# Optimization experiments

Hardware: AMD Instinct MI355X
Metric: run time of the kernel (lower is better)

The kernel has to match this reference:

```python
import jax, jax.numpy as jnp
import numpy as np

D = 256          # d_embed
KD = 256         # key_d_embed
NHEAD = 8
DK = D // NHEAD  # 32
QH = QW = 128
QWS = 16
KH = KW = 64
KWS = 8
R = QWS // KWS   # qk_ratio = 2
SCALE = 1.0 / np.sqrt(DK)


def _rel_index():
    # query coords on fine grid, key coords scaled up by ratio R
    qc = np.stack(np.meshgrid(np.arange(QWS), np.arange(QWS), indexing='ij'), -1).reshape(-1, 2)
    kc = np.stack(np.meshgrid(np.arange(KWS), np.arange(KWS), indexing='ij'), -1).reshape(-1, 2) * R
    rel = qc[:, None, :] - kc[None, :, :] + (QWS - R)  # values in [0, 2*QWS-R-1]
    return jnp.asarray(rel[..., 0] * (2 * QWS - R) + rel[..., 1])  # (QWS^2, KWS^2)


def _partition(t, ws):
    # (B, h, H, W, d) -> (B, h, H/ws, W/ws, ws*ws, d)
    B, h, H, W, d = t.shape
    t = t.reshape(B, h, H // ws, ws, W // ws, ws, d).transpose(0, 1, 2, 4, 3, 5, 6)
    return t.reshape(B, h, H // ws, W // ws, ws * ws, d)


def _merge(t, ws, H, W):
    # inverse of _partition
    B, h, nH, nW, _, d = t.shape
    t = t.reshape(B, h, nH, nW, ws, ws, d).transpose(0, 1, 2, 4, 3, 5, 6)
    return t.reshape(B, h, H, W, d)


def setup_inputs() -> dict:
    key = jax.random.key(0)
    ks = jax.random.split(key, 9)
    x = jax.random.normal(ks[0], (8, QH, QW, D), dtype=jnp.float32)
    z = jax.random.normal(ks[1], (8, KH, KW, KD), dtype=jnp.float32)
    mask = jax.random.randint(ks[2], (1, NHEAD, QH // QWS, QW // QWS, QWS * QWS, KWS * KWS), 0, 2) == 1
    Wq = jax.random.normal(ks[3], (D, D), dtype=jnp.float32) * 0.02
    bq = jnp.zeros((D,), dtype=jnp.float32)
    Wkv = jax.random.normal(ks[4], (KD, 2 * D), dtype=jnp.float32) * 0.02
    bkv = jnp.zeros((2 * D,), dtype=jnp.float32)
    Wo = jax.random.normal(ks[5], (D, D), dtype=jnp.float32) * 0.02
    bo = jnp.zeros((D,), dtype=jnp.float32)
    rel_table = jax.random.normal(ks[6], ((2 * QWS - R) ** 2, NHEAD), dtype=jnp.float32) * 0.02
    return {"x": x, "z": z, "mask": mask, "Wq": Wq, "bq": bq, "Wkv": Wkv, "bkv": bkv, "Wo": Wo, "bo": bo, "rel_table": rel_table}


def reference(x, z, mask, Wq, bq, Wkv, bkv, Wo, bo, rel_table):
    B, H, W, _ = x.shape
    q = (x @ Wq + bq).reshape(B, H, W, NHEAD, DK).transpose(0, 3, 1, 2, 4)        # (B,h,H,W,dk)
    kv = (z @ Wkv + bkv).reshape(B, KH, KW, 2, NHEAD, DK).transpose(3, 0, 4, 1, 2, 5)
    k, v = kv[0], kv[1]                                                           # (B,h,_H,_W,dk)
    sq, sk = QWS // 2, KWS // 2
    q = jnp.roll(q, (-sq, -sq), axis=(2, 3))
    k = jnp.roll(k, (-sk, -sk), axis=(2, 3))
    v = jnp.roll(v, (-sk, -sk), axis=(2, 3))
    q = _partition(q, QWS)   # (B,h,nh,nw,QWS^2,dk)
    k = _partition(k, KWS)   # (B,h,nh,nw,KWS^2,dk)
    v = _partition(v, KWS)
    attn = jnp.einsum('bhnmqd,bhnmkd->bhnmqk', q, k) * SCALE
    bias = rel_table[_rel_index()].transpose(2, 0, 1)[None, :, None, None]        # (1,h,1,1,QWS^2,KWS^2)
    attn = attn + bias
    attn = jnp.where(mask, jnp.float32(-1e9), attn)
    attn = jax.nn.softmax(attn, axis=-1)
    out = jnp.einsum('bhnmqk,bhnmkd->bhnmqd', attn, v)
    out = _merge(out, QWS, H, W)
    out = jnp.roll(out, (sq, sq), axis=(2, 3))
    out = out.transpose(0, 2, 3, 1, 4).reshape(B, H, W, D)
    return out @ Wo + bo
```

## Files before the change

kernel.cpp:

```cpp
#include <hip/hip_runtime.h>
#include <hip/hip_bf16.h>
#include <type_traits>


typedef __attribute__((ext_vector_type(8))) short short8v;
typedef __attribute__((ext_vector_type(4))) float f32x4;
typedef __attribute__((ext_vector_type(8))) unsigned short ushort8v;
typedef unsigned long long u64;

#define DEV __device__ __forceinline__

DEV unsigned short f2bf(float f) {
    union { float f; unsigned u; } v; v.f = f;
    unsigned r = v.u + 0x7FFFu + ((v.u >> 16) & 1u);
    return (unsigned short)(r >> 16);
}

DEV short8v cvt_f32x8(const float4 lo, const float4 hi) {
    union U { __hip_bfloat162 h[4]; short8v s; } u;
    u.h[0] = __float22bfloat162_rn(float2{lo.x, lo.y});
    u.h[1] = __float22bfloat162_rn(float2{lo.z, lo.w});
    u.h[2] = __float22bfloat162_rn(float2{hi.x, hi.y});
    u.h[3] = __float22bfloat162_rn(float2{hi.z, hi.w});
    return u.s;
}

DEV uint2 pack4(f32x4 v) {
    union { __hip_bfloat162 h; unsigned u; } a, b;
    a.h = __float22bfloat162_rn(float2{v[0], v[1]});
    b.h = __float22bfloat162_rn(float2{v[2], v[3]});
    return uint2{a.u, b.u};
}

#define ATT_SCALE 0.17677669529663687f

__global__ void prep_weights(const float* __restrict__ Wq, const float* __restrict__ Wkv,
                             const float* __restrict__ Wo,
                             unsigned short* __restrict__ WqT, unsigned short* __restrict__ WkvT,
                             unsigned short* __restrict__ WoT) {
    int idx = blockIdx.x * 256 + threadIdx.x;
    if (idx < 65536) {
        int n = idx >> 8, k = idx & 255;
        WqT[idx] = f2bf(Wq[k * 256 + n] * ATT_SCALE);
    } else if (idx < 196608) {
        int i = idx - 65536;
        int n = i >> 8, k = i & 255;
        WkvT[i] = f2bf(Wkv[k * 512 + n]);
    } else {
        int i = idx - 196608;
        int n = i >> 8, k = i & 255;
        WoT[i] = f2bf(Wo[k * 256 + n]);
    }
}

__global__ void prep_bias(const float* __restrict__ rel_table, const float* __restrict__ bq,
                          float* __restrict__ biasb, float* __restrict__ bqs) {
    int idx = blockIdx.x * 256 + threadIdx.x;
    if (idx < 131072) {
        int head = idx >> 14;
        int q = (idx >> 6) & 255;
        int k = idx & 63;
        int qi = q >> 4, qj = q & 15;
        int ki = k >> 3, kj = k & 7;
        int r0 = qi - 2 * ki + 14, r1 = qj - 2 * kj + 14;
        biasb[idx] = rel_table[(r0 * 30 + r1) * 8 + head];
    } else if (idx < 131328) {
        int i = idx - 131072;
        bqs[i] = bq[i] * ATT_SCALE;
    }
}

__global__ void prep_mask(const int* __restrict__ mask, u64* __restrict__ mp) {
    int idx = blockIdx.x * 256 + threadIdx.x;
    const int4* src = reinterpret_cast<const int4*>(mask + (size_t)idx * 64);
    u64 bits = 0;
#pragma unroll
    for (int c = 0; c < 16; ++c) {
        int4 v = src[c];
        if (v.x) bits |= 1ull << (c * 4 + 0);
        if (v.y) bits |= 1ull << (c * 4 + 1);
        if (v.z) bits |= 1ull << (c * 4 + 2);
        if (v.w) bits |= 1ull << (c * 4 + 3);
    }
    mp[idx] = bits;
}

__global__ __launch_bounds__(512, 2) void gemm_rs(
    const unsigned short* __restrict__ A,
    const unsigned short* __restrict__ WT,
    const float* __restrict__ bias, float* __restrict__ out)
{
    __shared__ __align__(16) unsigned char R[131072];

    const int tid = threadIdx.x;
    const int w = tid >> 6, lane = tid & 63, lr = lane & 15, lg = lane >> 4;
    const int g = w >> 2, wn = (w & 3) * 64;
    const size_t rowbase = (size_t)blockIdx.x * 512 + (size_t)g * 256;

    short8v wf[8][4];
#pragma unroll
    for (int kt = 0; kt < 8; ++kt)
#pragma unroll
        for (int nt = 0; nt < 4; ++nt)
            wf[kt][nt] = *reinterpret_cast<const short8v*>(
                WT + (size_t)(wn + nt * 16 + lr) * 256 + kt * 32 + lg * 8);

    const int r_ = lane >> 5;
    const int u_ = lane & 31;
    unsigned char* ringbase = R + w * 16384;
    const unsigned char* Ab = (const unsigned char*)A;

    auto issue = [&](int t, int slot) {
        size_t gbyte0 = (rowbase + (size_t)t * 16) * 512;
        unsigned char* ldst = ringbase + slot * 8192;
#pragma unroll
        for (int c = 0; c < 8; ++c) {
            int r = 2 * c + r_;
            int v = u_ ^ r;
            __builtin_amdgcn_global_load_lds(
                (const __attribute__((address_space(1))) void*)
                    (Ab + gbyte0 + (size_t)r * 512 + v * 16),
                (__attribute__((address_space(3))) void*)(ldst + c * 1024),
                16, 0, 0);
        }
    };

    issue(0, 0);

    for (int t = 0; t < 16; ++t) {
        const int slot = t & 1;
        if (t == 0) asm volatile("s_waitcnt vmcnt(0)" ::: "memory");
        else        asm volatile("s_waitcnt vmcnt(4)" ::: "memory");
        __builtin_amdgcn_sched_barrier(0);

        short8v af[8];
#pragma unroll
        for (int kt = 0; kt < 8; ++kt)
            af[kt] = *reinterpret_cast<const short8v*>(
                ringbase + slot * 8192 + lr * 512 + (((kt * 4 + lg) ^ lr) << 4));
        __builtin_amdgcn_sched_barrier(0);

        if (t + 1 < 16) issue(t + 1, slot ^ 1);

        f32x4 acc[4];
#pragma unroll
        for (int nt = 0; nt < 4; ++nt) acc[nt] = {0.f, 0.f, 0.f, 0.f};
#pragma unroll
        for (int kt = 0; kt < 8; ++kt)
#pragma unroll
            for (int nt = 0; nt < 4; ++nt)
                acc[nt] = __builtin_amdgcn_mfma_f32_16x16x32_bf16(
                    wf[kt][nt], af[kt], acc[nt], 0, 0, 0);

        size_t row = rowbase + (size_t)t * 16 + lr;
#pragma unroll
        for (int nt = 0; nt < 4; ++nt) {
            f32x4 b4 = *reinterpret_cast<const f32x4*>(bias + wn + nt * 16 + lg * 4);
            *reinterpret_cast<f32x4*>(out + row * 256 + wn + nt * 16 + lg * 4)
                = acc[nt] + b4;
        }
    }
}

template <bool AF32, bool OUT_BF16>
__global__ __launch_bounds__(512, 2) void gemm_ws(
    const void* __restrict__ Ain, const unsigned short* __restrict__ BT,
    const float* __restrict__ bias, void* __restrict__ Cout)
{
    __shared__ __align__(16) unsigned char Wl[131072];
    const float* Af = (const float*)Ain;

    const int tid = threadIdx.x;
    const int w = tid >> 6, lane = tid & 63, lr = lane & 15, lg = lane >> 4;
    const size_t wm = (size_t)blockIdx.x * 512 + w * 64;

    {
        int r = tid >> 1, half = tid & 1;
        const unsigned short* src = BT + r * 256 + half * 128;
        int rsw = (r >> 1) & 3;
#pragma unroll
        for (int kk = 0; kk < 4; ++kk) {
            int kt = half * 4 + kk;
#pragma unroll
            for (int sl = 0; sl < 4; ++sl) {
                ushort8v v = *reinterpret_cast<const ushort8v*>(src + kk * 32 + sl * 8);
                *reinterpret_cast<ushort8v*>(
                    &Wl[kt * 16384 + r * 64 + ((sl ^ rsw) << 4)]) = v;
            }
        }
    }
    __syncthreads();

    const int swzb = (lg ^ ((lr >> 1) & 3)) << 4;
    const int colb = lg * 4;

#define RD_W(kt, nt) (*reinterpret_cast<const short8v*>( \
        &Wl[(kt) * 16384 + ((nt) * 16 + lr) * 64 + swzb]))

#define EPILOGUE(t)                                                             \
    _Pragma("unroll")                                                           \
    for (int nt = 0; nt < 16; ++nt) {                                           \
        f32x4 b4 = *reinterpret_cast<const f32x4*>(bias + nt * 16 + colb);      \
        f32x4 v = acc[nt] + b4;                                                 \
        size_t row = wm + (t) * 16 + lr;                                        \
        if constexpr (OUT_BF16)                                                 \
            *reinterpret_cast<uint2*>(                                          \
                (unsigned short*)Cout + row * 256 + nt * 16 + colb) = pack4(v); \
        else                                                                    \
            *reinterpret_cast<f32x4*>(                                          \
                (float*)Cout + row * 256 + nt * 16 + colb) = v;                 \
    }

    float4 bufA[16], bufB[16];
#define LOADT_F(BUF, t) {                                                       \
        const float* p = Af + (wm + (t) * 16 + lr) * 256 + lg * 8;              \
        _Pragma("unroll")                                                       \
        for (int kt = 0; kt < 8; ++kt) {                                        \
            BUF[kt * 2]     = *reinterpret_cast<const float4*>(p + kt * 32);    \
            BUF[kt * 2 + 1] = *reinterpret_cast<const float4*>(p + kt * 32 + 4);\
        } }
#define COMP_F(BUF, t) {                                                        \
        f32x4 acc[16];                                                          \
        _Pragma("unroll")                                                       \
        for (int nt = 0; nt < 16; ++nt) acc[nt] = {0.f, 0.f, 0.f, 0.f};         \
        _Pragma("unroll")                                                       \
        for (int kt = 0; kt < 8; ++kt) {                                        \
            short8v a = cvt_f32x8(BUF[kt * 2], BUF[kt * 2 + 1]);                \
            _Pragma("unroll")                                                   \
            for (int nt = 0; nt < 16; ++nt)                                     \
                acc[nt] = __builtin_amdgcn_mfma_f32_16x16x32_bf16(              \
                    RD_W(kt, nt), a, acc[nt], 0, 0, 0);                         \
        }                                                                       \
        EPILOGUE(t) }
    LOADT_F(bufA, 0);
    LOADT_F(bufB, 1); COMP_F(bufA, 0);
    LOADT_F(bufA, 2); COMP_F(bufB, 1);
    LOADT_F(bufB, 3); COMP_F(bufA, 2);
    COMP_F(bufB, 3);
#undef LOADT_F
#undef COMP_F
#undef RD_W
#undef EPILOGUE
}

template <bool AF32, bool OUT_BF16>
__global__ __launch_bounds__(256) void gemm_proj(
    const void* __restrict__ Ain, const unsigned short* __restrict__ BT,
    const float* __restrict__ bias, void* __restrict__ Cout,
    int M, int N, int K)
{
    __shared__ __align__(16) unsigned char As[2][8192];
    __shared__ __align__(16) unsigned char Bs[2][8192];
    const float* Af = (const float*)Ain;

    const int tid = threadIdx.x;
    const int mb = blockIdx.y * 128, nb = blockIdx.x * 128;
    const int w = tid >> 6, lane = tid & 63, lr = lane & 15, lg = lane >> 4;
    const int wm = (w >> 1) * 64, wn = (w & 1) * 64;

    const int cr0 = (w << 5) + (lane >> 2);
    const int csp = lane & 3;
    const int cs0 = csp ^ ((cr0 >> 1) & 3);
    const int cs1 = csp ^ (((cr0 + 16) >> 1) & 3);

    auto stageB = [&](int buf, int kb) {
        __builtin_amdgcn_global_load_lds(
            (const __attribute__((address_space(1))) void*)(BT + (size_t)(nb + cr0) * K + kb + cs0 * 8),
            (__attribute__((address_space(3))) void*)(&Bs[buf][w << 11]), 16, 0, 0);
        __builtin_amdgcn_global_load_lds(
            (const __attribute__((address_space(1))) void*)(BT + (size_t)(nb + cr0 + 16) * K + kb + cs1 * 8),
            (__attribute__((address_space(3))) void*)(&Bs[buf][(w << 11) + 1024]), 16, 0, 0);
    };

    float4 areg[2][2];
    auto loadA = [&](int kb) {
#pragma unroll
        for (int i = 0; i < 2; ++i) {
            int flat = tid + (i << 8);
            int r = flat >> 2, sp = flat & 3;
            int s = sp ^ ((r >> 1) & 3);
            const float* src = Af + (size_t)(mb + r) * K + kb + s * 8;
            areg[i][0] = *reinterpret_cast<const float4*>(src);
            areg[i][1] = *reinterpret_cast<const float4*>(src + 4);
        }
    };
    auto writeA = [&](int buf) {
#pragma unroll
        for (int i = 0; i < 2; ++i) {
            int flat = tid + (i << 8);
            int r = flat >> 2, sp = flat & 3;
            ushort8v u = { f2bf(areg[i][0].x), f2bf(areg[i][0].y),
                           f2bf(areg[i][0].z), f2bf(areg[i][0].w),
                           f2bf(areg[i][1].x), f2bf(areg[i][1].y),
                           f2bf(areg[i][1].z), f2bf(areg[i][1].w) };
            *reinterpret_cast<ushort8v*>(&As[buf][r * 64 + sp * 16]) = u;
        }
    };
    auto rdA = [&](int buf, int row) -> short8v {
        int swz = (lg ^ ((row >> 1) & 3)) << 4;
        return *reinterpret_cast<const short8v*>(&As[buf][row * 64 + swz]);
    };
    auto rdB = [&](int buf, int row) -> short8v {
        int swz = (lg ^ ((row >> 1) & 3)) << 4;
        return *reinterpret_cast<const short8v*>(&Bs[buf][row * 64 + swz]);
    };

    f32x4 acc[4][4];
#pragma unroll
    for (int i = 0; i < 4; ++i)
#pragma unroll
        for (int j = 0; j < 4; ++j) acc[i][j] = {0.f, 0.f, 0.f, 0.f};

    loadA(0); stageB(0, 0); writeA(0);
    __syncthreads();

    const int NT = K >> 5;
    int cur = 0;
    for (int t = 0; t < NT; ++t) {
        if (t + 1 < NT) { loadA((t + 1) << 5); stageB(cur ^ 1, (t + 1) << 5); }
        short8v af[4], bfr[4];
#pragma unroll
        for (int mt = 0; mt < 4; ++mt) af[mt] = rdA(cur, wm + mt * 16 + lr);
#pragma unroll
        for (int nt = 0; nt < 4; ++nt) bfr[nt] = rdB(cur, wn + nt * 16 + lr);
#pragma unroll
        for (int mt = 0; mt < 4; ++mt)
#pragma unroll
            for (int nt = 0; nt < 4; ++nt)
                acc[mt][nt] = __builtin_amdgcn_mfma_f32_16x16x32_bf16(
                    af[mt], bfr[nt], acc[mt][nt], 0, 0, 0);
        if (t + 1 < NT) writeA(cur ^ 1);
        __syncthreads();
        cur ^= 1;
    }

#pragma unroll
    for (int mt = 0; mt < 4; ++mt)
#pragma unroll
        for (int nt = 0; nt < 4; ++nt)
#pragma unroll
            for (int j = 0; j < 4; ++j) {
                int row = mb + wm + mt * 16 + lg * 4 + j;
                int col = nb + wn + nt * 16 + lr;
                float v = acc[mt][nt][j] + bias[col];
                if constexpr (OUT_BF16)
                    ((unsigned short*)Cout)[(size_t)row * N + col] = f2bf(v);
                else
                    ((float*)Cout)[(size_t)row * N + col] = v;
            }
}

__global__ __launch_bounds__(256) void win_attn(
    unsigned short* __restrict__ Qbuf,
    const unsigned short* __restrict__ KVbuf,
    const u64* __restrict__ maskp,
    const float* __restrict__ biasb)
{
    __shared__ __align__(16) unsigned char Pb[256 * 128];
    __shared__ __align__(16) unsigned short Vt[32][72];

    const int tid = threadIdx.x;
    const int win = blockIdx.x, head = blockIdx.y, b = blockIdx.z;
    const int wi = win >> 3, wj = win & 7;
    const int w = tid >> 6, lane = tid & 63, lr = lane & 15, lg = lane >> 4;
    const int qb = w * 64;

    {
        int key = tid & 63, c = tid >> 6;
        int kr = (wi * 8 + (key >> 3) + 4) & 63;
        int kc = (wj * 8 + (key & 7) + 4) & 63;
        ushort8v v = *reinterpret_cast<const ushort8v*>(
            KVbuf + ((size_t)(b * 4096 + kr * 64 + kc)) * 512 + 256 + head * 32 + c * 8);
#pragma unroll
        for (int e = 0; e < 8; ++e) Vt[c * 8 + e][key] = v[e];
    }

    short8v qf[4], kf[4];
#pragma unroll
    for (int mt = 0; mt < 4; ++mt) {
        int q = qb + mt * 16 + lr;
        int gr = (wi * 16 + (q >> 4) + 8) & 127;
        int gc = (wj * 16 + (q & 15) + 8) & 127;
        qf[mt] = *reinterpret_cast<const short8v*>(
            Qbuf + ((size_t)(b * 16384 + gr * 128 + gc)) * 256 + head * 32 + lg * 8);
    }
#pragma unroll
    for (int nt = 0; nt < 4; ++nt) {
        int key = nt * 16 + lr;
        int kr = (wi * 8 + (key >> 3) + 4) & 63;
        int kc = (wj * 8 + (key & 7) + 4) & 63;
        kf[nt] = *reinterpret_cast<const short8v*>(
            KVbuf + ((size_t)(b * 4096 + kr * 64 + kc)) * 512 + head * 32 + lg * 8);
    }

    f32x4 s[4][4];
#pragma unroll
    for (int mt = 0; mt < 4; ++mt)
#pragma unroll
        for (int nt = 0; nt < 4; ++nt) s[mt][nt] = {0.f, 0.f, 0.f, 0.f};
    __builtin_amdgcn_s_setprio(1);
#pragma unroll
    for (int mt = 0; mt < 4; ++mt)
#pragma unroll
        for (int nt = 0; nt < 4; ++nt)
            s[mt][nt] = __builtin_amdgcn_mfma_f32_16x16x32_bf16(qf[mt], kf[nt], s[mt][nt], 0, 0, 0);
    __builtin_amdgcn_s_setprio(0);

    const u64* mrow = maskp + (size_t)(head * 64 + win) * 256;
#pragma unroll
    for (int mt = 0; mt < 4; ++mt) {
#pragma unroll
        for (int j = 0; j < 4; ++j) {
            int q = qb + mt * 16 + lg * 4 + j;
            u64 mb = mrow[q];
            const float* brow = biasb + (size_t)(head * 256 + q) * 64;
            float v[4];
            float m = -3.0e38f;
#pragma unroll
            for (int nt = 0; nt < 4; ++nt) {
                int key = nt * 16 + lr;
                float sv = s[mt][nt][j] + brow[key];
                if ((mb >> key) & 1ull) sv = -1.0e9f;
                v[nt] = sv;
                m = fmaxf(m, sv);
            }
#pragma unroll
            for (int d = 1; d < 16; d <<= 1) m = fmaxf(m, __shfl_xor(m, d, 64));
            float sum = 0.f;
#pragma unroll
            for (int nt = 0; nt < 4; ++nt) { v[nt] = __expf(v[nt] - m); sum += v[nt]; }
#pragma unroll
            for (int d = 1; d < 16; d <<= 1) sum += __shfl_xor(sum, d, 64);
            float inv = 1.0f / sum;
            int sw = (q & 7) << 4;
#pragma unroll
            for (int nt = 0; nt < 4; ++nt) {
                int off = q * 128 + (((nt * 16 + lr) * 2) ^ sw);
                *reinterpret_cast<unsigned short*>(Pb + off) = f2bf(v[nt] * inv);
            }
        }
    }

    __syncthreads();

    f32x4 o[4][2];
#pragma unroll
    for (int mt = 0; mt < 4; ++mt)
#pragma unroll
        for (int nt = 0; nt < 2; ++nt) o[mt][nt] = {0.f, 0.f, 0.f, 0.f};
#pragma unroll
    for (int kc = 0; kc < 2; ++kc) {
        short8v pf[4], vf[2];
#pragma unroll
        for (int mt = 0; mt < 4; ++mt) {
            int row = qb + mt * 16 + lr;
            int coff = (kc * 64 + lg * 16) ^ ((row & 7) << 4);
            pf[mt] = *reinterpret_cast<const short8v*>(Pb + row * 128 + coff);
        }
#pragma unroll
        for (int nt = 0; nt < 2; ++nt)
            vf[nt] = *reinterpret_cast<const short8v*>(&Vt[nt * 16 + lr][kc * 32 + lg * 8]);
        __builtin_amdgcn_s_setprio(1);
#pragma unroll
        for (int mt = 0; mt < 4; ++mt)
#pragma unroll
            for (int nt = 0; nt < 2; ++nt)
                o[mt][nt] = __builtin_amdgcn_mfma_f32_16x16x32_bf16(pf[mt], vf[nt], o[mt][nt], 0, 0, 0);
        __builtin_amdgcn_s_setprio(0);
    }

#pragma unroll
    for (int mt = 0; mt < 4; ++mt)
#pragma unroll
        for (int j = 0; j < 4; ++j) {
            int q = qb + mt * 16 + lg * 4 + j;
            int gr = (wi * 16 + (q >> 4) + 8) & 127;
            int gc = (wj * 16 + (q & 15) + 8) & 127;
            unsigned short* dst =
                Qbuf + ((size_t)(b * 16384 + gr * 128 + gc)) * 256 + head * 32;
#pragma unroll
            for (int nt = 0; nt < 2; ++nt)
                dst[nt * 16 + lr] = f2bf(o[mt][nt][j]);
        }
}

extern "C" void kernel_launch(void* const* d_in, const int* in_sizes, int n_in,
                              void* d_out, int out_size, void* d_ws, size_t ws_size,
                              hipStream_t stream) {
    const float* x    = (const float*)d_in[0];
    const float* z    = (const float*)d_in[1];
    const int*   mask = (const int*)d_in[2];
    const float* Wq   = (const float*)d_in[3];
    const float* bq   = (const float*)d_in[4];
    const float* Wkv  = (const float*)d_in[5];
    const float* bkv  = (const float*)d_in[6];
    const float* Wo   = (const float*)d_in[7];
    const float* bo   = (const float*)d_in[8];
    const float* rel  = (const float*)d_in[9];
    float* out = (float*)d_out;

    char* ws = (char*)d_ws;
    unsigned short* Qbuf  = (unsigned short*)(ws);
    unsigned short* KVbuf = (unsigned short*)(ws + 67108864);
    unsigned short* WqT   = (unsigned short*)(ws + 100663296);
    unsigned short* WkvT  = (unsigned short*)(ws + 100794368);
    unsigned short* WoT   = (unsigned short*)(ws + 101056512);
    float*          biasb = (float*)(ws + 101187584);
    u64*            maskp = (u64*)(ws + 101711872);
    float*          bqs   = (float*)(ws + 102760448);

    prep_weights<<<1024, 256, 0, stream>>>(Wq, Wkv, Wo, WqT, WkvT, WoT);
    prep_bias<<<513, 256, 0, stream>>>(rel, bq, biasb, bqs);
    prep_mask<<<512, 256, 0, stream>>>(mask, maskp);

    gemm_ws<true, true><<<256, 512, 0, stream>>>(
        (const void*)x, WqT, bqs, (void*)Qbuf);
    gemm_proj<true, true><<<dim3(4, 256), 256, 0, stream>>>(
        (const void*)z, WkvT, bkv, (void*)KVbuf, 32768, 512, 256);
    win_attn<<<dim3(64, 8, 8), 256, 0, stream>>>(Qbuf, KVbuf, maskp, biasb);
    gemm_rs<<<256, 512, 0, stream>>>(Qbuf, WoT, bo, out);
}
```

Baseline: 219.2 us.

## Replace Q projection GEMM with register-stationary weights and async LDS-staged A loads

The Q projection GEMM now holds each wave's 64-column weight slice in registers and streams fp32 activation rows through a double-buffered per-wave LDS ring filled by global_load_lds direct copies. It uses an XOR swizzle to avoid bank conflicts and waits on vmcnt so loads overlap the MFMA work. This replaces the previous kernel, which staged the full weight matrix in LDS and loaded A tiles through registers. The new kernel uses 256 threads with one block per CU and a 128KB LDS footprint, which may limit occupancy and latency hiding.

```diff
diff --git a/kernel.cpp b/kernel.cpp
--- a/kernel.cpp
+++ b/kernel.cpp
@@ -85,6 +85,85 @@
     mp[idx] = bits;
 }
 
+__global__ __launch_bounds__(256, 1) void gemm_qrs(
+    const float* __restrict__ A,
+    const unsigned short* __restrict__ WT,
+    const float* __restrict__ bias,
+    unsigned short* __restrict__ Cout)
+{
+    __shared__ __align__(16) unsigned char R[131072];
+
+    const int tid = threadIdx.x;
+    const int w = tid >> 6, lane = tid & 63, lr = lane & 15, lg = lane >> 4;
+    const int wn = w * 64;
+    const size_t rowbase = (size_t)blockIdx.x * 512;
+
+    short8v wf[8][4];
+#pragma unroll
+    for (int kt = 0; kt < 8; ++kt)
+#pragma unroll
+        for (int nt = 0; nt < 4; ++nt)
+            wf[kt][nt] = *reinterpret_cast<const short8v*>(
+                WT + (size_t)(wn + nt * 16 + lr) * 256 + kt * 32 + lg * 8);
+
+    unsigned char* ringbase = R + w * 32768;
+    const unsigned char* Ab = (const unsigned char*)A;
+
+    auto issue = [&](int t, int slot) {
+        size_t gbyte0 = (rowbase + (size_t)t * 16) * 1024;
+        unsigned char* ldst = ringbase + slot * 16384;
+#pragma unroll
+        for (int r = 0; r < 16; ++r) {
+            int v = lane ^ r;
+            __builtin_amdgcn_global_load_lds(
+                (const __attribute__((address_space(1))) void*)
+                    (Ab + gbyte0 + (size_t)r * 1024 + (size_t)v * 16),
+                (__attribute__((address_space(3))) void*)(ldst + r * 1024),
+                16, 0, 0);
+        }
+    };
+
+    issue(0, 0);
+
+    for (int t = 0; t < 32; ++t) {
+        const int slot = t & 1;
+        if (t == 0) asm volatile("s_waitcnt vmcnt(0)" ::: "memory");
+        else        asm volatile("s_waitcnt vmcnt(4)" ::: "memory");
+        __builtin_amdgcn_sched_barrier(0);
+
+        short8v af[8];
+#pragma unroll
+        for (int kt = 0; kt < 8; ++kt) {
+            int U0 = kt * 8 + lg * 2;
+            const unsigned char* base = ringbase + slot * 16384 + lr * 1024;
+            float4 f0 = *reinterpret_cast<const float4*>(base + ((U0 ^ lr) << 4));
+            float4 f1 = *reinterpret_cast<const float4*>(base + (((U0 + 1) ^ lr) << 4));
+            af[kt] = cvt_f32x8(f0, f1);
+        }
+        __builtin_amdgcn_sched_barrier(0);
+
+        if (t + 1 < 32) issue(t + 1, slot ^ 1);
+
+        f32x4 acc[4];
+#pragma unroll
+        for (int nt = 0; nt < 4; ++nt) acc[nt] = {0.f, 0.f, 0.f, 0.f};
+#pragma unroll
+        for (int kt = 0; kt < 8; ++kt)
+#pragma unroll
+            for (int nt = 0; nt < 4; ++nt)
+                acc[nt] = __builtin_amdgcn_mfma_f32_16x16x32_bf16(
+                    wf[kt][nt], af[kt], acc[nt], 0, 0, 0);
+
+        size_t row = rowbase + (size_t)t * 16 + lr;
+#pragma unroll
+        for (int nt = 0; nt < 4; ++nt) {
+            f32x4 b4 = *reinterpret_cast<const f32x4*>(bias + wn + nt * 16 + lg * 4);
+            *reinterpret_cast<uint2*>(
+                Cout + row * 256 + wn + nt * 16 + lg * 4) = pack4(acc[nt] + b4);
+        }
+    }
+}
+
 __global__ __launch_bounds__(512, 2) void gemm_rs(
     const unsigned short* __restrict__ A,
     const unsigned short* __restrict__ WT,
@@ -160,87 +239,6 @@
                 = acc[nt] + b4;
         }
     }
-}
-
-template <bool AF32, bool OUT_BF16>
-__global__ __launch_bounds__(512, 2) void gemm_ws(
-    const void* __restrict__ Ain, const unsigned short* __restrict__ BT,
-    const float* __restrict__ bias, void* __restrict__ Cout)
-{
-    __shared__ __align__(16) unsigned char Wl[131072];
-    const float* Af = (const float*)Ain;
-
-    const int tid = threadIdx.x;
-    const int w = tid >> 6, lane = tid & 63, lr = lane & 15, lg = lane >> 4;
-    const size_t wm = (size_t)blockIdx.x * 512 + w * 64;
-
-    {
-        int r = tid >> 1, half = tid & 1;
-        const unsigned short* src = BT + r * 256 + half * 128;
-        int rsw = (r >> 1) & 3;
-#pragma unroll
-        for (int kk = 0; kk < 4; ++kk) {
-            int kt = half * 4 + kk;
-#pragma unroll
-            for (int sl = 0; sl < 4; ++sl) {
-                ushort8v v = *reinterpret_cast<const ushort8v*>(src + kk * 32 + sl * 8);
-                *reinterpret_cast<ushort8v*>(
-                    &Wl[kt * 16384 + r * 64 + ((sl ^ rsw) << 4)]) = v;
-            }
-        }
-    }
-    __syncthreads();
-
-    const int swzb = (lg ^ ((lr >> 1) & 3)) << 4;
-    const int colb = lg * 4;
-
-#define RD_W(kt, nt) (*reinterpret_cast<const short8v*>( \
-        &Wl[(kt) * 16384 + ((nt) * 16 + lr) * 64 + swzb]))
-
-#define EPILOGUE(t)                                                             \
-    _Pragma("unroll")                                                           \
-    for (int nt = 0; nt < 16; ++nt) {                                           \
-        f32x4 b4 = *reinterpret_cast<const f32x4*>(bias + nt * 16 + colb);      \
-        f32x4 v = acc[nt] + b4;                                                 \
-        size_t row = wm + (t) * 16 + lr;                                        \
-        if constexpr (OUT_BF16)                                                 \
-            *reinterpret_cast<uint2*>(                                          \
-                (unsigned short*)Cout + row * 256 + nt * 16 + colb) = pack4(v); \
-        else                                                                    \
-            *reinterpret_cast<f32x4*>(                                          \
-                (float*)Cout + row * 256 + nt * 16 + colb) = v;                 \
-    }
-
-    float4 bufA[16], bufB[16];
-#define LOADT_F(BUF, t) {                                                       \
-        const float* p = Af + (wm + (t) * 16 + lr) * 256 + lg * 8;              \
-        _Pragma("unroll")                                                       \
-        for (int kt = 0; kt < 8; ++kt) {                                        \
-            BUF[kt * 2]     = *reinterpret_cast<const float4*>(p + kt * 32);    \
-            BUF[kt * 2 + 1] = *reinterpret_cast<const float4*>(p + kt * 32 + 4);\
-        } }
-#define COMP_F(BUF, t) {                                                        \
-        f32x4 acc[16];                                                          \
-        _Pragma("unroll")                                                       \
-        for (int nt = 0; nt < 16; ++nt) acc[nt] = {0.f, 0.f, 0.f, 0.f};         \
-        _Pragma("unroll")                                                       \
-        for (int kt = 0; kt < 8; ++kt) {                                        \
-            short8v a = cvt_f32x8(BUF[kt * 2], BUF[kt * 2 + 1]);                \
-            _Pragma("unroll")                                                   \
-            for (int nt = 0; nt < 16; ++nt)                                     \
-                acc[nt] = __builtin_amdgcn_mfma_f32_16x16x32_bf16(              \
-                    RD_W(kt, nt), a, acc[nt], 0, 0, 0);                         \
-        }                                                                       \
-        EPILOGUE(t) }
-    LOADT_F(bufA, 0);
-    LOADT_F(bufB, 1); COMP_F(bufA, 0);
-    LOADT_F(bufA, 2); COMP_F(bufB, 1);
-    LOADT_F(bufB, 3); COMP_F(bufA, 2);
-    COMP_F(bufB, 3);
-#undef LOADT_F
-#undef COMP_F
-#undef RD_W
-#undef EPILOGUE
 }
 
 template <bool AF32, bool OUT_BF16>
@@ -513,8 +511,7 @@
     prep_bias<<<513, 256, 0, stream>>>(rel, bq, biasb, bqs);
     prep_mask<<<512, 256, 0, stream>>>(mask, maskp);
 
-    gemm_ws<true, true><<<256, 512, 0, stream>>>(
-        (const void*)x, WqT, bqs, (void*)Qbuf);
+    gemm_qrs<<<256, 256, 0, stream>>>(x, WqT, bqs, Qbuf);
     gemm_proj<true, true><<<dim3(4, 256), 256, 0, stream>>>(
         (const void*)z, WkvT, bkv, (void*)KVbuf, 32768, 512, 256);
     win_attn<<<dim3(64, 8, 8), 256, 0, stream>>>(Qbuf, KVbuf, maskp, biasb);
```

Result: slower. 232.4 us (+6.0%).
